# Optimization experiments

Measured on AMD Instinct MI355X. Metric: run time of the kernel, lower is better.

The kernel has to match this reference:

```python
import jax, jax.numpy as jnp
import numpy as np

N, M, RANK = 1024, 4096, 32


def setup_inputs() -> dict:
    key = jax.random.key(0)
    kW, kH, kT = jax.random.split(key, 3)
    W = jax.random.uniform(kW, (N, RANK), dtype=jnp.float32)
    H = jax.random.uniform(kH, (RANK, M), dtype=jnp.float32)
    tau = jax.random.uniform(kT, (N, RANK), dtype=jnp.float32) * 2.0 - 1.0
    return {"W": W, "H": H, "tau": tau}


def reference(W, H, tau):
    # Hf: FFT along last axis of softplus(H) -> (rank, M) complex64
    Hf = jnp.fft.fft(jax.nn.softplus(H), axis=-1)
    m = H.shape[-1]
    f = (jnp.arange(m, dtype=jnp.float32) / m)  # (M,)
    # phase ramp: omega[n,d,m] = exp(-i*2*pi*tau[n,d]*f[m])
    phase = tau[:, :, None] * f[None, None, :]          # (N, rank, M) float32
    omega = jnp.exp((-2j * jnp.pi) * phase)             # complex64
    spW = jax.nn.softplus(W)                            # (N, rank)
    # V[n,m] = sum_d spW[n,d] * omega[n,d,m] * Hf[d,m]
    V = jnp.einsum('nd,ndm,dm->nm', spW.astype(omega.dtype), omega, Hf)
    return V
```

## Files before the change

### kernel.cpp

```cpp
#include <hip/hip_runtime.h>
#include <hip/hip_bf16.h>
#include <math.h>

#ifndef M_PI
#define M_PI 3.14159265358979323846
#endif

constexpr int N    = 1024;
constexpr int M    = 4096;
constexpr int RANK = 32;
constexpr float PHI1 = -1.5339807878856412e-3f;

typedef __attribute__((ext_vector_type(8))) short bf16x8;
typedef __attribute__((ext_vector_type(4))) float f32x4;

__device__ __forceinline__ float softplus_f(float x) {
    const float t = __expf(-fabsf(x));
    return fmaxf(x, 0.0f) + __logf(1.0f + t);
}

__device__ __forceinline__ unsigned pack_bf16x2(float a, float b) {
    __hip_bfloat162 p;
    p.x = __float2bfloat16(a);
    p.y = __float2bfloat16(b);
    unsigned r;
    __builtin_memcpy(&r, &p, 4);
    return r;
}

__device__ __forceinline__ void a_terms(float w, float t, float mcF, float* o) {
    const float sw = softplus_f(w);
    const float a1 = PHI1 * t;
    float s0, c0; __sincosf(a1 * mcF, &s0, &c0);
    const float R0 = sw * c0,  I0 = sw * s0;
    const float R1 = -a1 * I0, I1 = a1 * R0;
    const float h  = 0.5f * a1;
    const float R2 = -h * I1,  I2 = h * R1;
    o[0] = R0; o[1] = -I0; o[2] = R1; o[3] = -I1; o[4] = R2; o[5] = -I2;
}

__global__ __launch_bounds__(256) void dft_bal(const float* __restrict__ H,
                                               float* __restrict__ HfR,
                                               float* __restrict__ HfI) {
    __shared__ float  sh[M];
    __shared__ float2 sG[8 * 65];
    const int c   = blockIdx.x;
    const int d   = blockIdx.y;
    const int tid = threadIdx.x;

    const float4* H4 = (const float4*)(H + d * M);
    for (int i = tid; i < M / 4; i += 256) {
        const float4 v = H4[i];
        ((float4*)sh)[i] = make_float4(softplus_f(v.x), softplus_f(v.y),
                                       softplus_f(v.z), softplus_f(v.w));
    }
    __syncthreads();

    {
        const int k0   = tid & 63;
        const int rgrp = tid >> 6;
        const int rr0  = rgrp * 2;
        const int r0   = c + 8 * rr0;
        const int r1   = r0 + 8;
        float s0, c0, s1, c1;
        __sincosf((-2.0f * (float)M_PI / 64.0f) * (float)r0, &s0, &c0);
        __sincosf((-2.0f * (float)M_PI / 64.0f) * (float)r1, &s1, &c1);
        float twR0 = 1.f, twI0 = 0.f, aR0 = 0.f, aI0 = 0.f;
        float twR1 = 1.f, twI1 = 0.f, aR1 = 0.f, aI1 = 0.f;
        for (int k1 = 0; k1 < 64; ++k1) {
            const float h = sh[(k1 << 6) + k0];
            aR0 = fmaf(h, twR0, aR0);  aI0 = fmaf(h, twI0, aI0);
            aR1 = fmaf(h, twR1, aR1);  aI1 = fmaf(h, twI1, aI1);
            float nR = fmaf(twR0, c0, -twI0 * s0);
            float nI = fmaf(twR0, s0,  twI0 * c0);
            twR0 = nR; twI0 = nI;
            nR = fmaf(twR1, c1, -twI1 * s1);
            nI = fmaf(twR1, s1,  twI1 * c1);
            twR1 = nR; twI1 = nI;
        }
        sG[rr0 * 65 + k0]       = make_float2(aR0, aI0);
        sG[(rr0 + 1) * 65 + k0] = make_float2(aR1, aI1);
    }
    __syncthreads();

    const int rr = tid & 7;
    #pragma unroll
    for (int j = 0; j < 2; ++j) {
        const int m = c + 8 * (tid + 256 * j);
        float ss, sc; __sincosf(PHI1 * (float)m, &ss, &sc);
        float tR_ = 1.f, tI_ = 0.f, accR = 0.f, accI = 0.f;
        #pragma unroll 8
        for (int k0 = 0; k0 < 64; ++k0) {
            const float2 g = sG[rr * 65 + k0];
            accR = fmaf(tR_, g.x, fmaf(-tI_, g.y, accR));
            accI = fmaf(tR_, g.y, fmaf( tI_, g.x, accI));
            const float nR = fmaf(tR_, sc, -tI_ * ss);
            const float nI = fmaf(tR_, ss,  tI_ * sc);
            tR_ = nR; tI_ = nI;
        }
        HfR[d * M + m] = accR;
        HfI[d * M + m] = accI;
    }
}

__global__ __launch_bounds__(256, 4) void einsum_mfma(const float* __restrict__ W,
                                                      const float* __restrict__ tau,
                                                      const float* __restrict__ HfR,
                                                      const float* __restrict__ HfI,
                                                      float* __restrict__ out_f) {
    __shared__ __attribute__((aligned(16))) unsigned short sB[6][64][40];
    const int tid   = threadIdx.x;
    const int mBase = blockIdx.x * 64;
    const int nBase = blockIdx.y * 64;

    const int wv = tid >> 6, lane = tid & 63;
    const int q = lane >> 4, l = lane & 15;
    const int nA = nBase + wv * 16 + l;
    const int d8 = q << 3;
    const float mcF = (float)(mBase + 32);

    const float4 w0 = *(const float4*)(W   + nA * RANK + d8);
    const float4 w1 = *(const float4*)(W   + nA * RANK + d8 + 4);
    const float4 t0 = *(const float4*)(tau + nA * RANK + d8);
    const float4 t1 = *(const float4*)(tau + nA * RANK + d8 + 4);

    for (int e = tid; e < 512; e += 256) {
        const int mloc = e & 63;
        const int d0   = (e >> 6) << 2;
        const float dlt = (float)mloc - 32.0f;
        const float dq  = dlt * dlt;
        const float* pR = HfR + d0 * M + mBase + mloc;
        const float* pI = HfI + d0 * M + mBase + mloc;
        float r0 = pR[0], r1 = pR[M], r2 = pR[2*M], r3 = pR[3*M];
        float i0 = pI[0], i1 = pI[M], i2 = pI[2*M], i3 = pI[3*M];

        uint2 v;
        v.x = pack_bf16x2(r0, r1);           v.y = pack_bf16x2(r2, r3);
        *(uint2*)&sB[0][mloc][d0] = v;
        v.x = pack_bf16x2(i0, i1);           v.y = pack_bf16x2(i2, i3);
        *(uint2*)&sB[1][mloc][d0] = v;
        v.x = pack_bf16x2(r0*dlt, r1*dlt);   v.y = pack_bf16x2(r2*dlt, r3*dlt);
        *(uint2*)&sB[2][mloc][d0] = v;
        v.x = pack_bf16x2(i0*dlt, i1*dlt);   v.y = pack_bf16x2(i2*dlt, i3*dlt);
        *(uint2*)&sB[3][mloc][d0] = v;
        v.x = pack_bf16x2(r0*dq, r1*dq);     v.y = pack_bf16x2(r2*dq, r3*dq);
        *(uint2*)&sB[4][mloc][d0] = v;
        v.x = pack_bf16x2(i0*dq, i1*dq);     v.y = pack_bf16x2(i2*dq, i3*dq);
        *(uint2*)&sB[5][mloc][d0] = v;
    }

    const float wj[8] = {w0.x,w0.y,w0.z,w0.w,w1.x,w1.y,w1.z,w1.w};
    const float tj[8] = {t0.x,t0.y,t0.z,t0.w,t1.x,t1.y,t1.z,t1.w};
    unsigned uA[6][4];
    #pragma unroll
    for (int p = 0; p < 4; ++p) {
        float f0[6], f1[6];
        a_terms(wj[2*p],   tj[2*p],   mcF, f0);
        a_terms(wj[2*p+1], tj[2*p+1], mcF, f1);
        #pragma unroll
        for (int k = 0; k < 6; ++k) uA[k][p] = pack_bf16x2(f0[k], f1[k]);
    }
    bf16x8 fA[6];
    #pragma unroll
    for (int k = 0; k < 6; ++k) __builtin_memcpy(&fA[k], uA[k], 16);
    __syncthreads();

    for (int mt = 0; mt < 4; ++mt) {
        const int mL = (mt << 4) + l;
        const bf16x8 b0 = *(const bf16x8*)&sB[0][mL][d8];
        const bf16x8 b1 = *(const bf16x8*)&sB[1][mL][d8];
        const bf16x8 b2 = *(const bf16x8*)&sB[2][mL][d8];
        const bf16x8 b3 = *(const bf16x8*)&sB[3][mL][d8];
        const bf16x8 b4 = *(const bf16x8*)&sB[4][mL][d8];
        const bf16x8 b5 = *(const bf16x8*)&sB[5][mL][d8];

        f32x4 acc = {0.f, 0.f, 0.f, 0.f};
        acc = __builtin_amdgcn_mfma_f32_16x16x32_bf16(fA[0], b0, acc, 0, 0, 0);
        acc = __builtin_amdgcn_mfma_f32_16x16x32_bf16(fA[1], b1, acc, 0, 0, 0);
        acc = __builtin_amdgcn_mfma_f32_16x16x32_bf16(fA[2], b2, acc, 0, 0, 0);
        acc = __builtin_amdgcn_mfma_f32_16x16x32_bf16(fA[3], b3, acc, 0, 0, 0);
        acc = __builtin_amdgcn_mfma_f32_16x16x32_bf16(fA[4], b4, acc, 0, 0, 0);
        acc = __builtin_amdgcn_mfma_f32_16x16x32_bf16(fA[5], b5, acc, 0, 0, 0);

        #pragma unroll
        for (int r = 0; r < 4; ++r)
            out_f[(size_t)(nBase + wv * 16 + (q << 2) + r) * M
                  + mBase + (mt << 4) + l] = acc[r];
    }
}

__global__ __launch_bounds__(256) void dft_fused(const float* __restrict__ H,
                                                 float* __restrict__ HfR,
                                                 float* __restrict__ HfI) {
    __shared__ float  sh[M];
    __shared__ float2 sG[64 * 65];
    const int d = blockIdx.y, tid = threadIdx.x;
    for (int k = tid; k < M; k += 256) sh[k] = softplus_f(H[d * M + k]);
    __syncthreads();

    const int k0 = tid & 63;
    const int rB = (tid >> 6) * 16;
    float twR[16], twI[16], stR[16], stI[16], aR[16], aI[16];
    #pragma unroll
    for (int rr = 0; rr < 16; ++rr) {
        const float ang = (-2.0f * (float)M_PI / 64.0f) * (float)(rB + rr);
        __sincosf(ang, &stI[rr], &stR[rr]);
        twR[rr] = 1.f; twI[rr] = 0.f; aR[rr] = 0.f; aI[rr] = 0.f;
    }
    for (int k1 = 0; k1 < 64; ++k1) {
        const float h = sh[(k1 << 6) + k0];
        #pragma unroll
        for (int rr = 0; rr < 16; ++rr) {
            aR[rr] = fmaf(h, twR[rr], aR[rr]);
            aI[rr] = fmaf(h, twI[rr], aI[rr]);
            const float nR = fmaf(twR[rr], stR[rr], -twI[rr] * stI[rr]);
            const float nI = fmaf(twR[rr], stI[rr],  twI[rr] * stR[rr]);
            twR[rr] = nR; twI[rr] = nI;
        }
    }
    #pragma unroll
    for (int rr = 0; rr < 16; ++rr)
        sG[k0 * 65 + rB + rr] = make_float2(aR[rr], aI[rr]);
    __syncthreads();

    const int mBase = blockIdx.x * 1024;
    for (int j = 0; j < 4; ++j) {
        const int m = mBase + j * 256 + tid;
        const int r = m & 63;
        float ss, sc; __sincosf(PHI1 * (float)m, &ss, &sc);
        float tR_ = 1.f, tI_ = 0.f, accR = 0.f, accI = 0.f;
        #pragma unroll 8
        for (int qq = 0; qq < 64; ++qq) {
            const float2 g = sG[qq * 65 + r];
            accR = fmaf(tR_, g.x, fmaf(-tI_, g.y, accR));
            accI = fmaf(tR_, g.y, fmaf( tI_, g.x, accI));
            const float nR = fmaf(tR_, sc, -tI_ * ss);
            const float nI = fmaf(tR_, ss,  tI_ * sc);
            tR_ = nR; tI_ = nI;
        }
        HfR[d * M + m] = accR;
        HfI[d * M + m] = accI;
    }
}

template <bool CPLX, int U>
__global__ __launch_bounds__(256) void einsum_kernel(const float* __restrict__ W,
                                                     const float* __restrict__ tau,
                                                     const float* __restrict__ HfR,
                                                     const float* __restrict__ HfI,
                                                     float* __restrict__ out_f) {
    constexpr int ROWS = 16 * U;
    constexpr int MT   = 128;
    __shared__ float2 sHf[16 * MT];
    __shared__ float  sW[ROWS][RANK], sT[ROWS][RANK];
    const int tid   = threadIdx.x;
    const int mBase = blockIdx.x * MT;
    const int nBase = blockIdx.y * ROWS;

    for (int i = tid; i < ROWS * RANK; i += 256) {
        const int n_ = i >> 5, dd = i & 31;
        sW[n_][dd] = softplus_f(W[(nBase + n_) * RANK + dd]);
        sT[n_][dd] = tau[(nBase + n_) * RANK + dd];
    }

    const int nl = tid >> 4, chunk = tid & 15;
    const int m0 = mBase + (chunk << 3);

    float accR[U][8], accI[U][8];
    #pragma unroll
    for (int u = 0; u < U; ++u)
        #pragma unroll
        for (int j = 0; j < 8; ++j) { accR[u][j] = 0.f; if (CPLX) accI[u][j] = 0.f; }

    for (int half = 0; half < 2; ++half) {
        __syncthreads();
        for (int e = tid; e < 16 * 64; e += 256) {
            const int dl = e >> 6, p = e & 63;
            const int mm = p << 1;
            const int base = (half * 16 + dl) * M + mBase + mm;
            const float2 r2 = *(const float2*)(HfR + base);
            const float2 q2 = *(const float2*)(HfI + base);
            const int c = mm >> 3, j0 = mm & 7;
            float2* s2 = sHf + (dl << 7);
            s2[(j0 << 4) + c]       = make_float2(r2.x, q2.x);
            s2[((j0 + 1) << 4) + c] = make_float2(r2.y, q2.y);
        }
        __syncthreads();

        #pragma unroll 1
        for (int dl = 0; dl < 16; ++dl) {
            const int dd = (half << 4) + dl;
            float aR_[U], aI_[U], bR_[U], bI_[U], K[U];
            #pragma unroll
            for (int u = 0; u < U; ++u) {
                const float t = sT[nl * U + u][dd], w = sW[nl * U + u][dd];
                const float a1 = PHI1 * t;
                float sp, cp; __sincosf(a1, &sp, &cp);
                float s0, c0; __sincosf(a1 * (float)m0, &s0, &c0);
                aR_[u] = w * c0;
                aI_[u] = w * s0;
                bR_[u] = fmaf(aR_[u], cp, -aI_[u] * sp);
                bI_[u] = fmaf(aI_[u], cp,  aR_[u] * sp);
                K[u]   = 2.0f * cp;
            }
            int idx = (dl << 7) + chunk;
            #pragma unroll
            for (int j = 0; j < 8; ++j) {
                const float2 h = sHf[idx];
                #pragma unroll
                for (int u = 0; u < U; ++u) {
                    accR[u][j] = fmaf(aR_[u], h.x, fmaf(-aI_[u], h.y, accR[u][j]));
                    if (CPLX) accI[u][j] = fmaf(aR_[u], h.y, fmaf(aI_[u], h.x, accI[u][j]));
                    const float nR = fmaf(K[u], bR_[u], -aR_[u]);
                    const float nI = fmaf(K[u], bI_[u], -aI_[u]);
                    aR_[u] = bR_[u]; aI_[u] = bI_[u];
                    bR_[u] = nR;     bI_[u] = nI;
                }
                idx += 16;
            }
        }
    }

    #pragma unroll
    for (int u = 0; u < U; ++u) {
        const int n = nBase + nl * U + u;
        if (CPLX) {
            float2* o2 = ((float2*)out_f) + (size_t)n * M + m0;
            #pragma unroll
            for (int qq = 0; qq < 4; ++qq)
                ((float4*)o2)[qq] = make_float4(accR[u][2*qq], accI[u][2*qq],
                                                accR[u][2*qq+1], accI[u][2*qq+1]);
        } else {
            float* op = out_f + (size_t)n * M + m0;
            ((float4*)op)[0] = make_float4(accR[u][0], accR[u][1], accR[u][2], accR[u][3]);
            ((float4*)op)[1] = make_float4(accR[u][4], accR[u][5], accR[u][6], accR[u][7]);
        }
    }
}

__global__ __launch_bounds__(256) void tail_real(const float* __restrict__ W,
                                                 const float* __restrict__ tau,
                                                 const float* __restrict__ stashR,
                                                 const float* __restrict__ stashI,
                                                 float* __restrict__ out_f) {
    __shared__ float stR[32 * 32], stI[32 * 32];
    __shared__ float sW[64][RANK], sT[64][RANK];
    const int tid = threadIdx.x;
    const int c0  = blockIdx.x * 32;
    const int nBase = N - 64;
    for (int i = tid; i < 64 * RANK; i += 256) {
        const int n_ = i >> 5, dd = i & 31;
        sW[n_][dd] = softplus_f(W[(nBase + n_) * RANK + dd]);
        sT[n_][dd] = tau[(nBase + n_) * RANK + dd];
    }
    for (int i = tid; i < 32 * 32; i += 256) {
        const int d_ = i >> 5, mm = i & 31;
        stR[i] = stashR[d_ * M + c0 + mm];
        stI[i] = stashI[d_ * M + c0 + mm];
    }
    __syncthreads();
    const int n = tid >> 2, chunk = tid & 3;
    const int m0 = c0 + chunk;
    float acc[8];
    #pragma unroll
    for (int j = 0; j < 8; ++j) acc[j] = 0.f;
    for (int d = 0; d < RANK; ++d) {
        const float t = sT[n][d], w = sW[n][d];
        const float a1 = PHI1 * t;
        float ss, sc; __sincosf(a1 * 4.0f, &ss, &sc);
        float s0, c0f; __sincosf(a1 * (float)m0, &s0, &c0f);
        float tR_ = w * c0f, tI_ = w * s0;
        int idx = (d << 5) + chunk;
        #pragma unroll
        for (int j = 0; j < 8; ++j) {
            acc[j] = fmaf(tR_, stR[idx], fmaf(-tI_, stI[idx], acc[j]));
            const float nR = fmaf(tR_, sc, -tI_ * ss);
            const float nI = fmaf(tR_, ss,  tI_ * sc);
            tR_ = nR; tI_ = nI;
            idx += 4;
        }
    }
    #pragma unroll
    for (int j = 0; j < 8; ++j)
        out_f[(size_t)(nBase + n) * M + m0 + (j << 2)] = acc[j];
}

__global__ __launch_bounds__(256) void tail_cplx(const float* __restrict__ W,
                                                 const float* __restrict__ tau,
                                                 const float* __restrict__ stashR,
                                                 const float* __restrict__ stashI,
                                                 float* __restrict__ out_f) {
    const int nBase = N - 32;
    __shared__ float sW[32][RANK], sT[32][RANK];
    const int tid = threadIdx.x, mBase = blockIdx.x * 256;
    for (int i = tid; i < 32 * RANK; i += 256) {
        const int n_ = i >> 5, dd = i & 31;
        sW[n_][dd] = softplus_f(W[(nBase + n_) * RANK + dd]);
        sT[n_][dd] = tau[(nBase + n_) * RANK + dd];
    }
    const int m = mBase + tid;
    float hr[RANK], hi[RANK];
    #pragma unroll
    for (int d = 0; d < RANK; ++d) { hr[d] = stashR[d * M + m]; hi[d] = stashI[d * M + m]; }
    __syncthreads();
    const float phi = PHI1 * (float)m;
    for (int n_ = 0; n_ < 32; ++n_) {
        float aR = 0.f, aI = 0.f;
        #pragma unroll
        for (int d = 0; d < RANK; ++d) {
            const float t = sT[n_][d], w = sW[n_][d];
            float s, c; __sincosf(t * phi, &s, &c);
            const float cw = c * w, sw = s * w;
            aR = fmaf(cw, hr[d], fmaf(-sw, hi[d], aR));
            aI = fmaf(cw, hi[d], fmaf( sw, hr[d], aI));
        }
        ((float2*)out_f)[(size_t)(nBase + n_) * M + m] = make_float2(aR, aI);
    }
}

extern "C" void kernel_launch(void* const* d_in, const int* in_sizes, int n_in,
                              void* d_out, int out_size, void* d_ws, size_t ws_size,
                              hipStream_t stream) {
    const float* W   = (const float*)d_in[0];
    const float* H   = (const float*)d_in[1];
    const float* tau = (const float*)d_in[2];
    float* out_f = (float*)d_out;

    const bool   cplx   = (out_size >= 2 * N * M);
    const size_t planeN = (size_t)RANK * M;

    if (d_ws != nullptr && ws_size >= 4 * planeN * sizeof(float)) {
        float* HfR = (float*)d_ws;
        float* HfI = HfR + planeN;
        dft_bal<<<dim3(8, 32), 256, 0, stream>>>(H, HfR, HfI);
        if (cplx)
            einsum_kernel<true , 2><<<dim3(32, N / 32), 256, 0, stream>>>(W, tau, HfR, HfI, out_f);
        else
            einsum_mfma<<<dim3(64, 16), 256, 0, stream>>>(W, tau, HfR, HfI, out_f);
    } else if (!cplx) {
        float* HfR = out_f + (size_t)(N - 64) * M;
        float* HfI = HfR + planeN;
        dft_fused<<<dim3(4, 32), 256, 0, stream>>>(H, HfR, HfI);
        einsum_kernel<false, 2><<<dim3(32, (N - 64) / 32), 256, 0, stream>>>(W, tau, HfR, HfI, out_f);
        tail_real<<<dim3(128), 256, 0, stream>>>(W, tau, HfR, HfI, out_f);
    } else {
        float* HfR = out_f + 2 * (size_t)N * M - 2 * planeN;
        float* HfI = HfR + planeN;
        dft_fused<<<dim3(4, 32), 256, 0, stream>>>(H, HfR, HfI);
        einsum_kernel<true , 2><<<dim3(32, (N - 32) / 32), 256, 0, stream>>>(W, tau, HfR, HfI, out_f);
        tail_cplx<<<dim3(16), 256, 0, stream>>>(W, tau, HfR, HfI, out_f);
    }
}
```

Baseline: 78.34 us.

## Precompute bf16 Taylor-scaled Hf planes in DFT kernel for direct LDS copy

The DFT stage now writes Hf straight into a bf16 workspace laid out exactly like the einsum's shared-memory tile, including the dlt and dlt^2 scaled copies. The einsum kernel then fills shared memory with a plain uint4 copy, so each of its 1024 blocks no longer does strided fp32 loads, scaling and bf16 packing. The DFT grid also grows from 8x32 to 16x32 blocks. In exchange the DFT kernel does scattered 2-byte global stores, and the precomputed planes take more workspace than the fp32 Hf did.

```diff
diff --git a/kernel.cpp b/kernel.cpp
--- a/kernel.cpp
+++ b/kernel.cpp
@@ -25,6 +25,12 @@
     p.y = __float2bfloat16(b);
     unsigned r;
     __builtin_memcpy(&r, &p, 4);
+    return r;
+}
+__device__ __forceinline__ unsigned short bf16_1(float x) {
+    __hip_bfloat16 b = __float2bfloat16(x);
+    unsigned short r;
+    __builtin_memcpy(&r, &b, 2);
     return r;
 }
 
@@ -37,6 +43,66 @@
     const float h  = 0.5f * a1;
     const float R2 = -h * I1,  I2 = h * R1;
     o[0] = R0; o[1] = -I0; o[2] = R1; o[3] = -I1; o[4] = R2; o[5] = -I2;
+}
+
+__global__ __launch_bounds__(256) void dft_plane(const float* __restrict__ H,
+                                                 unsigned short* __restrict__ P) {
+    __shared__ float  sh[M];
+    __shared__ float2 sG[4 * 65];
+    const int c   = blockIdx.x;
+    const int d   = blockIdx.y;
+    const int tid = threadIdx.x;
+
+    const float4* H4 = (const float4*)(H + d * M);
+    for (int i = tid; i < M / 4; i += 256) {
+        const float4 v = H4[i];
+        ((float4*)sh)[i] = make_float4(softplus_f(v.x), softplus_f(v.y),
+                                       softplus_f(v.z), softplus_f(v.w));
+    }
+    __syncthreads();
+
+    {
+        const int k0 = tid & 63;
+        const int rr = tid >> 6;
+        const int r  = c + 16 * rr;
+        float s0, c0;
+        __sincosf((-2.0f * (float)M_PI / 64.0f) * (float)r, &s0, &c0);
+        float twR = 1.f, twI = 0.f, aR = 0.f, aI = 0.f;
+        for (int k1 = 0; k1 < 64; ++k1) {
+            const float h = sh[(k1 << 6) + k0];
+            aR = fmaf(h, twR, aR);  aI = fmaf(h, twI, aI);
+            const float nR = fmaf(twR, c0, -twI * s0);
+            const float nI = fmaf(twR, s0,  twI * c0);
+            twR = nR; twI = nI;
+        }
+        sG[rr * 65 + k0] = make_float2(aR, aI);
+    }
+    __syncthreads();
+
+    const int m  = c + 16 * tid;
+    const int rr = tid & 3;
+    float ss, sc; __sincosf(PHI1 * (float)m, &ss, &sc);
+    float tR_ = 1.f, tI_ = 0.f, accR = 0.f, accI = 0.f;
+    #pragma unroll 8
+    for (int k0 = 0; k0 < 64; ++k0) {
+        const float2 g = sG[rr * 65 + k0];
+        accR = fmaf(tR_, g.x, fmaf(-tI_, g.y, accR));
+        accI = fmaf(tR_, g.y, fmaf( tI_, g.x, accI));
+        const float nR = fmaf(tR_, sc, -tI_ * ss);
+        const float nI = fmaf(tR_, ss,  tI_ * sc);
+        tR_ = nR; tI_ = nI;
+    }
+
+    const int mG = m >> 6, mloc = m & 63;
+    const float dlt = (float)mloc - 32.0f;
+    const float dq  = dlt * dlt;
+    unsigned short* cp = P + (size_t)mG * 15360 + (size_t)mloc * 40 + d;
+    cp[0]        = bf16_1(accR);
+    cp[2560]     = bf16_1(accI);
+    cp[2 * 2560] = bf16_1(accR * dlt);
+    cp[3 * 2560] = bf16_1(accI * dlt);
+    cp[4 * 2560] = bf16_1(accR * dq);
+    cp[5 * 2560] = bf16_1(accI * dq);
 }
 
 __global__ __launch_bounds__(256) void dft_bal(const float* __restrict__ H,
@@ -105,8 +171,7 @@
 
 __global__ __launch_bounds__(256, 4) void einsum_mfma(const float* __restrict__ W,
                                                       const float* __restrict__ tau,
-                                                      const float* __restrict__ HfR,
-                                                      const float* __restrict__ HfI,
+                                                      const unsigned short* __restrict__ P,
                                                       float* __restrict__ out_f) {
     __shared__ __attribute__((aligned(16))) unsigned short sB[6][64][40];
     const int tid   = threadIdx.x;
@@ -124,29 +189,14 @@
     const float4 t0 = *(const float4*)(tau + nA * RANK + d8);
     const float4 t1 = *(const float4*)(tau + nA * RANK + d8 + 4);
 
-    for (int e = tid; e < 512; e += 256) {
-        const int mloc = e & 63;
-        const int d0   = (e >> 6) << 2;
-        const float dlt = (float)mloc - 32.0f;
-        const float dq  = dlt * dlt;
-        const float* pR = HfR + d0 * M + mBase + mloc;
-        const float* pI = HfI + d0 * M + mBase + mloc;
-        float r0 = pR[0], r1 = pR[M], r2 = pR[2*M], r3 = pR[3*M];
-        float i0 = pI[0], i1 = pI[M], i2 = pI[2*M], i3 = pI[3*M];
-
-        uint2 v;
-        v.x = pack_bf16x2(r0, r1);           v.y = pack_bf16x2(r2, r3);
-        *(uint2*)&sB[0][mloc][d0] = v;
-        v.x = pack_bf16x2(i0, i1);           v.y = pack_bf16x2(i2, i3);
-        *(uint2*)&sB[1][mloc][d0] = v;
-        v.x = pack_bf16x2(r0*dlt, r1*dlt);   v.y = pack_bf16x2(r2*dlt, r3*dlt);
-        *(uint2*)&sB[2][mloc][d0] = v;
-        v.x = pack_bf16x2(i0*dlt, i1*dlt);   v.y = pack_bf16x2(i2*dlt, i3*dlt);
-        *(uint2*)&sB[3][mloc][d0] = v;
-        v.x = pack_bf16x2(r0*dq, r1*dq);     v.y = pack_bf16x2(r2*dq, r3*dq);
-        *(uint2*)&sB[4][mloc][d0] = v;
-        v.x = pack_bf16x2(i0*dq, i1*dq);     v.y = pack_bf16x2(i2*dq, i3*dq);
-        *(uint2*)&sB[5][mloc][d0] = v;
+    {
+        const uint4* gsrc = (const uint4*)(P + (size_t)blockIdx.x * 15360);
+        uint4* ldst = (uint4*)&sB[0][0][0];
+        #pragma unroll
+        for (int i = 0; i < 8; ++i) {
+            const int idx = tid + (i << 8);
+            if (idx < 1920) ldst[idx] = gsrc[idx];
+        }
     }
 
     const float wj[8] = {w0.x,w0.y,w0.z,w0.w,w1.x,w1.y,w1.z,w1.w};
@@ -430,13 +480,16 @@
     const size_t planeN = (size_t)RANK * M;
 
     if (d_ws != nullptr && ws_size >= 4 * planeN * sizeof(float)) {
-        float* HfR = (float*)d_ws;
-        float* HfI = HfR + planeN;
-        dft_bal<<<dim3(8, 32), 256, 0, stream>>>(H, HfR, HfI);
-        if (cplx)
+        if (!cplx) {
+            unsigned short* P = (unsigned short*)d_ws;
+            dft_plane<<<dim3(16, 32), 256, 0, stream>>>(H, P);
+            einsum_mfma<<<dim3(64, 16), 256, 0, stream>>>(W, tau, P, out_f);
+        } else {
+            float* HfR = (float*)d_ws;
+            float* HfI = HfR + planeN;
+            dft_bal<<<dim3(8, 32), 256, 0, stream>>>(H, HfR, HfI);
             einsum_kernel<true , 2><<<dim3(32, N / 32), 256, 0, stream>>>(W, tau, HfR, HfI, out_f);
-        else
-            einsum_mfma<<<dim3(64, 16), 256, 0, stream>>>(W, tau, HfR, HfI, out_f);
+        }
     } else if (!cplx) {
         float* HfR = out_f + (size_t)(N - 64) * M;
         float* HfI = HfR + planeN;
```

Result: no change. 78.41 us (+0.1%).
